# Performance work log

Measured on AMD Instinct MI355X. Metric: run time of the kernel, lower is better.

The kernel has to match this reference:

```python
import jax, jax.numpy as jnp
import numpy as np

N, E, F_IN, H, C = 50000, 800000, 128, 64, 10

def setup_inputs() -> dict:
    key = jax.random.key(0)
    ks = jax.random.split(key, 8)
    x = jax.random.normal(ks[0], (N, F_IN), dtype=jnp.float32)
    edge_index = jax.random.randint(ks[1], (2, E), 0, N, dtype=jnp.int32)
    edge_weight = jax.random.uniform(ks[2], (E,), dtype=jnp.float32)
    W1 = jax.random.normal(ks[3], (H, F_IN), dtype=jnp.float32) * 0.05
    W2 = jax.random.normal(ks[4], (H, H), dtype=jnp.float32) * 0.05
    W3 = jax.random.normal(ks[5], (C, H), dtype=jnp.float32) * 0.05
    b1 = jnp.zeros((H,), jnp.float32)
    b2 = jnp.zeros((H,), jnp.float32)
    b3 = jnp.zeros((C,), jnp.float32)
    return {"x": x, "edge_index": edge_index, "edge_weight": edge_weight,
            "W1": W1, "b1": b1, "W2": W2, "b2": b2, "W3": W3, "b3": b3}

def reference(x, edge_index, edge_weight, W1, b1, W2, b2, W3, b3):
    n = x.shape[0]
    row, col = edge_index[0], edge_index[1]
    # GCN symmetric normalization (add_self_loops=False): deg from edge weights on col
    deg = jax.ops.segment_sum(edge_weight, col, num_segments=n)  # [N]
    dinv = jnp.where(deg > 0, jax.lax.rsqrt(deg), 0.0)
    norm = dinv[row] * edge_weight * dinv[col]  # [E]

    def gcn_layer(h, W, b):
        h = h @ W.T                               # linear transform [N, out]
        msg = h[row] * norm[:, None]              # gather + scale   [E, out]
        agg = jax.ops.segment_sum(msg, col, num_segments=n)  # scatter-add [N, out]
        return agg + b

    h = gcn_layer(x, W1, b1)
    h = gcn_layer(h, W2, b2)
    logits = gcn_layer(h, W3, b3)
    soft = jax.nn.softmax(logits, axis=1)
    return logits, soft
```

## Files before the change

kernel.cpp:

```cpp
#include <hip/hip_runtime.h>
#include <hip/hip_fp16.h>

#define N_NODES 50000
#define N_EDGES 800000
#define F_IN    128
#define H_DIM   64
#define C_DIM   10
#define CPAD    16
#define CAP     48
#define BLOCK   256
#define BIN_NODES 256
#define NBINS   196
#define STRIDE  4480
#define E_BLK   2048
#define ABLOCKS ((N_EDGES + E_BLK - 1) / E_BLK)
#define DGB     (N_NODES / 16)
#define WB      ((N_NODES * 64) / 256)
#define POISON  ((int)0xAAAAAAAA)

__device__ __forceinline__ int unbase(int v) {
    return ((unsigned)v < 65536u) ? v : v - POISON;
}

__device__ __forceinline__ int   prow(unsigned v) { return (int)(v >> 16); }
__device__ __forceinline__ float pw(unsigned v)   {
    return __half2float(__ushort_as_half((unsigned short)(v & 0xFFFFu)));
}

__global__ __launch_bounds__(256) void k_binA(const int* __restrict__ rows,
                                              const int* __restrict__ cols,
                                              const float* __restrict__ ew,
                                              const float* __restrict__ W1,
                                              const float* __restrict__ b1,
                                              const float* __restrict__ W2,
                                              const float* __restrict__ b2,
                                              const float* __restrict__ W3,
                                              int* __restrict__ bucketCnt,
                                              unsigned* __restrict__ regionA,
                                              unsigned short* __restrict__ regionC,
                                              float* __restrict__ T2g,
                                              float* __restrict__ v1g,
                                              float* __restrict__ v2g) {
    const int tid = threadIdx.x;
    if (blockIdx.x < ABLOCKS) {
        __shared__ unsigned       sA[E_BLK];
        __shared__ unsigned short sC[E_BLK];
        __shared__ int hcnt[NBINS];
        __shared__ int lbase[NBINS];
        __shared__ int gb[NBINS];
        for (int i = tid; i < NBINS; i += BLOCK) hcnt[i] = 0;
        __syncthreads();

        const int e0 = blockIdx.x * E_BLK;
        unsigned rw[8];
        unsigned cl[8];
#pragma unroll
        for (int j = 0; j < 8; ++j) {
            int e = e0 + j * BLOCK + tid;
            if (e < N_EDGES) {
                int   c = cols[e];
                int   r = rows[e];
                float w = ew[e];
                rw[j] = ((unsigned)r << 16) | (unsigned)__half_as_ushort(__float2half(w));
                int lr = atomicAdd(&hcnt[c >> 8], 1);
                cl[j] = (unsigned)c | ((unsigned)lr << 16);
            } else {
                cl[j] = 0xFFFFFFFFu;
            }
        }
        __syncthreads();

        if (tid < 64) {
            int run = 0;
            for (int base = 0; base < NBINS; base += 64) {
                int i = base + tid;
                int v = (i < NBINS) ? hcnt[i] : 0;
                int s = v;
#pragma unroll
                for (int off = 1; off < 64; off <<= 1) {
                    int t = __shfl_up(s, off);
                    if (tid >= off) s += t;
                }
                if (i < NBINS) lbase[i] = run + s - v;
                run += __shfl(s, 63);
            }
        }
        __syncthreads();

#pragma unroll
        for (int j = 0; j < 8; ++j) {
            if (cl[j] != 0xFFFFFFFFu) {
                int c  = (int)(cl[j] & 0xFFFFu);
                int lr = (int)(cl[j] >> 16);
                int pos = lbase[c >> 8] + lr;
                sA[pos] = rw[j];
                sC[pos] = (unsigned short)c;
            }
        }
        if (tid < NBINS) gb[tid] = unbase(atomicAdd(&bucketCnt[tid], hcnt[tid]));
        __syncthreads();

        const int total = lbase[NBINS - 1] + hcnt[NBINS - 1];
        for (int i = tid; i < total; i += BLOCK) {
            int c = sC[i];
            int b = c >> 8;
            int gpos = gb[b] + (i - lbase[b]);
            if (gpos < STRIDE) {
                size_t p = (size_t)b * STRIDE + gpos;
                regionA[p] = sA[i];
                regionC[p] = (unsigned short)c;
            }
        }
        return;
    }

    __shared__ float u[C_DIM * H_DIM];
    for (int idx = tid; idx < C_DIM * H_DIM; idx += BLOCK) {
        int c = idx >> 6, j = idx & 63;
        float a = 0.f;
#pragma unroll
        for (int k = 0; k < H_DIM; ++k) a += W3[c * H_DIM + k] * W2[k * H_DIM + j];
        u[idx] = a;
    }
    __syncthreads();
    for (int idx = tid; idx < C_DIM * F_IN; idx += BLOCK) {
        int c = idx >> 7, f = idx & 127;
        float a = 0.f;
#pragma unroll
        for (int k = 0; k < H_DIM; ++k) a += u[c * H_DIM + k] * W1[k * F_IN + f];
        T2g[idx] = a;
    }
    if (tid < C_DIM) {
        float a = 0.f, b = 0.f;
#pragma unroll
        for (int k = 0; k < H_DIM; ++k) {
            a += u[tid * H_DIM + k] * b1[k];
            b += W3[tid * H_DIM + k] * b2[k];
        }
        v1g[tid] = a;
        v2g[tid] = b;
    }
}

__global__ __launch_bounds__(256) void k_binB(const int* __restrict__ bucketCnt,
                                              const unsigned* __restrict__ regionA,
                                              const unsigned short* __restrict__ regionC,
                                              float2* __restrict__ meta,
                                              unsigned* __restrict__ edata) {
    __shared__ unsigned sdata[BIN_NODES * CAP];
    __shared__ int   lcnt[BIN_NODES];
    __shared__ float wsum[BIN_NODES];
    const int tid = threadIdx.x;
    const int b   = blockIdx.x;
    if (tid < BIN_NODES) { lcnt[tid] = 0; wsum[tid] = 0.f; }
    __syncthreads();

    int tot = unbase(bucketCnt[b]);
    if (tot > STRIDE) tot = STRIDE;
    const size_t segBase = (size_t)b * STRIDE;
    for (int i = tid; i < tot; i += BLOCK) {
        unsigned e = regionA[segBase + i];
        int nl = (int)regionC[segBase + i] - b * BIN_NODES;
        int r = atomicAdd(&lcnt[nl], 1);
        if (r < CAP) sdata[nl * CAP + r] = e;
        atomicAdd(&wsum[nl], pw(e));
    }
    __syncthreads();

    const int n0 = b * BIN_NODES;
    const int nvalid = min(N_NODES - n0, BIN_NODES);
    if (tid < nvalid) {
        int c0 = min(lcnt[tid], CAP);
        int cp = (c0 + 15) & ~15;
        if (cp > CAP) cp = CAP;
        for (int r = c0; r < cp; ++r) sdata[tid * CAP + r] = 0u;
        float d = wsum[tid];
        meta[n0 + tid] = make_float2(d > 0.f ? rsqrtf(d) : 0.f, (float)cp);
    }
    __syncthreads();

    int4* dst = reinterpret_cast<int4*>(edata + (size_t)n0 * CAP);
    const int4* src = reinterpret_cast<const int4*>(sdata);
    const int nvec = nvalid * CAP / 4;
    for (int i = tid; i < nvec; i += BLOCK) dst[i] = src[i];
}

__global__ __launch_bounds__(256) void k_dg(const float* __restrict__ x,
                                            const float* __restrict__ T2g,
                                            const float2* __restrict__ meta,
                                            __half* __restrict__ bufA) {
    __shared__ float ts[16 * 132];
    __shared__ float xs[16][132];
    const int tid = threadIdx.x;
    const int n0 = blockIdx.x * 16;

    for (int i = tid; i < 16 * F_IN; i += BLOCK) {
        int c = i >> 7;
        ts[c * 132 + (i & 127)] = (c < C_DIM) ? T2g[i] : 0.f;
    }
    for (int i = tid; i < 16 * 32; i += BLOCK) {
        int ln = i >> 5, f4 = i & 31;
        float4 v = reinterpret_cast<const float4*>(x)[(n0 + ln) * 32 + f4];
        *reinterpret_cast<float4*>(&xs[ln][f4 * 4]) = v;
    }
    __syncthreads();

    const int g = tid >> 4;
    const int c = tid & 15;
    const int n = n0 + g;
    const float di = meta[n].x;

    const float4* tsv = reinterpret_cast<const float4*>(&ts[c * 132]);
    const float4* xv  = reinterpret_cast<const float4*>(&xs[g][0]);
    float a = 0.f;
#pragma unroll 8
    for (int f4 = 0; f4 < 32; ++f4) {
        float4 xx = xv[f4], tt = tsv[f4];
        a += xx.x * tt.x + xx.y * tt.y + xx.z * tt.z + xx.w * tt.w;
    }
    float outv = (c < C_DIM) ? a * di : (c == 10 ? di : 0.f);
    bufA[n * CPAD + c] = __float2half(outv);
}

__global__ __launch_bounds__(256) void k_gather(const float2* __restrict__ meta,
                                                const unsigned* __restrict__ edata,
                                                const __half* __restrict__ zin,
                                                __half* __restrict__ zout) {
    int n = (blockIdx.x * 256 + threadIdx.x) >> 6;
    if (n >= N_NODES) return;
    int lane = threadIdx.x & 63;
    int sub = lane >> 4, c = lane & 15;
    float2 m = meta[n];
    float di = m.x;
    int iters = ((int)m.y) >> 4;
    int base = n * CAP + sub;
    float acc = 0.f;
#pragma unroll
    for (int i = 0; i < 3; ++i) {
        if (i < iters) {
            int k = base + i * 16;
            unsigned e0 = edata[k];
            unsigned e1 = edata[k + 4];
            unsigned e2 = edata[k + 8];
            unsigned e3 = edata[k + 12];
            acc += pw(e0) * __half2float(zin[prow(e0) * CPAD + c]);
            acc += pw(e1) * __half2float(zin[prow(e1) * CPAD + c]);
            acc += pw(e2) * __half2float(zin[prow(e2) * CPAD + c]);
            acc += pw(e3) * __half2float(zin[prow(e3) * CPAD + c]);
        }
    }
    acc += __shfl_xor(acc, 32);
    acc += __shfl_xor(acc, 16);
    if (lane < 16) zout[n * CPAD + lane] = __float2half(acc * di * di);
}

__global__ __launch_bounds__(256) void k_final(const float2* __restrict__ meta,
                                               const unsigned* __restrict__ edata,
                                               const __half* __restrict__ zin,
                                               const __half* __restrict__ s1buf,
                                               const float* __restrict__ v1,
                                               const float* __restrict__ v2,
                                               const float* __restrict__ b3,
                                               float* __restrict__ logits,
                                               float* __restrict__ soft) {
    int n = (blockIdx.x * 256 + threadIdx.x) >> 6;
    if (n >= N_NODES) return;
    int lane = threadIdx.x & 63;
    int sub = lane >> 4, c = lane & 15;
    float2 m = meta[n];
    float di = m.x;
    int iters = ((int)m.y) >> 4;
    int base = n * CAP + sub;
    float acc = 0.f;
#pragma unroll
    for (int i = 0; i < 3; ++i) {
        if (i < iters) {
            int k = base + i * 16;
            unsigned e0 = edata[k];
            unsigned e1 = edata[k + 4];
            unsigned e2 = edata[k + 8];
            unsigned e3 = edata[k + 12];
            acc += pw(e0) * __half2float(zin[prow(e0) * CPAD + c]);
            acc += pw(e1) * __half2float(zin[prow(e1) * CPAD + c]);
            acc += pw(e2) * __half2float(zin[prow(e2) * CPAD + c]);
            acc += pw(e3) * __half2float(zin[prow(e3) * CPAD + c]);
        }
    }
    acc += __shfl_xor(acc, 32);
    acc += __shfl_xor(acc, 16);

    float r  = di > 0.f ? 1.0f / di : 0.f;
    float a1 = __half2float(s1buf[n * CPAD + 10]) * r;
    float a2 = __half2float(zin[n * CPAD + 10]) * r;
    float l = (c < C_DIM) ? di * acc + a2 * v1[c] + a1 * v2[c] + b3[c] : -1e30f;
    float mx = l;
#pragma unroll
    for (int d = 8; d >= 1; d >>= 1) mx = fmaxf(mx, __shfl_xor(mx, d));
    float ev = (c < C_DIM) ? __expf(l - mx) : 0.f;
    float s = ev;
#pragma unroll
    for (int d = 8; d >= 1; d >>= 1) s += __shfl_xor(s, d);
    if (lane < C_DIM) {
        logits[n * C_DIM + lane] = l;
        soft[n * C_DIM + lane]   = ev / s;
    }
}

extern "C" void kernel_launch(void* const* d_in, const int* in_sizes, int n_in,
                              void* d_out, int out_size, void* d_ws, size_t ws_size,
                              hipStream_t stream) {
    const float* x  = (const float*)d_in[0];
    const int*   ei = (const int*)d_in[1];
    const float* ew = (const float*)d_in[2];
    const float* W1 = (const float*)d_in[3];
    const float* b1 = (const float*)d_in[4];
    const float* W2 = (const float*)d_in[5];
    const float* b2 = (const float*)d_in[6];
    const float* W3 = (const float*)d_in[7];
    const float* b3 = (const float*)d_in[8];
    const int* rows = ei;
    const int* cols = ei + N_EDGES;

    char* ws = (char*)d_ws;
    size_t off = 0;
    auto alloc = [&](size_t bytes) { void* q = ws + off; off += (bytes + 15) & ~size_t(15); return q; };

    float2*         meta      = (float2*)         alloc((size_t)N_NODES * 8);
    __half*         bufA      = (__half*)         alloc((size_t)N_NODES * CPAD * 2);
    __half*         bufB      = (__half*)         alloc((size_t)N_NODES * CPAD * 2);
    float*          T2g       = (float*)          alloc(C_DIM * F_IN * 4);
    float*          v1        = (float*)          alloc(64);
    float*          v2        = (float*)          alloc(64);
    int*            bucketCnt = (int*)            alloc(NBINS * 4);
    unsigned*       regionA   = (unsigned*)       alloc((size_t)NBINS * STRIDE * 4);
    unsigned short* regionC   = (unsigned short*) alloc((size_t)NBINS * STRIDE * 2);
    unsigned*       edata     = (unsigned*)       alloc((size_t)N_NODES * CAP * 4);

    float* logits = (float*)d_out;
    float* soft   = logits + N_NODES * C_DIM;

    k_binA<<<ABLOCKS + 1, 256, 0, stream>>>(rows, cols, ew, W1, b1, W2, b2, W3,
                                            bucketCnt, regionA, regionC, T2g, v1, v2);
    k_binB<<<NBINS, 256, 0, stream>>>(bucketCnt, regionA, regionC, meta, edata);
    k_dg<<<DGB, 256, 0, stream>>>(x, T2g, meta, bufA);
    k_gather<<<WB, 256, 0, stream>>>(meta, edata, bufA, bufB);
    k_gather<<<WB, 256, 0, stream>>>(meta, edata, bufB, bufA);
    k_final<<<WB, 256, 0, stream>>>(meta, edata, bufA, bufB, v1, v2, b3,
                                    logits, soft);
}
```

Measured before the change: 166.7 us.

## Split binB into quarter-bin blocks and vectorize gather with half2 loads

The bucket-compaction kernel now launches four blocks per bin. Each block scans the whole bin but keeps only the 64 nodes in its quarter, which raises parallelism and shrinks shared memory per block at the cost of reading each bin's data four times. The gather and final kernels switch to 8 edge lanes × 8 half2 feature lanes, with uint2 edge loads and a three-step shuffle reduction, which halves the scalar zin loads. The final softmax now writes float2 pairs. It also skips the bucket atomic when a bin's local count is zero.

```diff
diff --git a/kernel.cpp b/kernel.cpp
--- a/kernel.cpp
+++ b/kernel.cpp
@@ -11,6 +11,7 @@
 #define BLOCK   256
 #define BIN_NODES 256
 #define NBINS   196
+#define QN      64
 #define STRIDE  4480
 #define E_BLK   2048
 #define ABLOCKS ((N_EDGES + E_BLK - 1) / E_BLK)
@@ -97,7 +98,8 @@
                 sC[pos] = (unsigned short)c;
             }
         }
-        if (tid < NBINS) gb[tid] = unbase(atomicAdd(&bucketCnt[tid], hcnt[tid]));
+        if (tid < NBINS && hcnt[tid] > 0)
+            gb[tid] = unbase(atomicAdd(&bucketCnt[tid], hcnt[tid]));
         __syncthreads();
 
         const int total = lbase[NBINS - 1] + hcnt[NBINS - 1];
@@ -147,28 +149,34 @@
                                               const unsigned short* __restrict__ regionC,
                                               float2* __restrict__ meta,
                                               unsigned* __restrict__ edata) {
-    __shared__ unsigned sdata[BIN_NODES * CAP];
-    __shared__ int   lcnt[BIN_NODES];
-    __shared__ float wsum[BIN_NODES];
+    __shared__ unsigned sdata[QN * CAP];
+    __shared__ int   lcnt[QN];
+    __shared__ float wsum[QN];
     const int tid = threadIdx.x;
-    const int b   = blockIdx.x;
-    if (tid < BIN_NODES) { lcnt[tid] = 0; wsum[tid] = 0.f; }
+    const int b   = blockIdx.x >> 2;
+    const int q   = blockIdx.x & 3;
+    const int n0  = b * BIN_NODES + q * QN;
+    if (n0 >= N_NODES) return;
+    if (tid < QN) { lcnt[tid] = 0; wsum[tid] = 0.f; }
     __syncthreads();
 
     int tot = unbase(bucketCnt[b]);
     if (tot > STRIDE) tot = STRIDE;
     const size_t segBase = (size_t)b * STRIDE;
+    const int lo = q * QN, hi = lo + QN;
     for (int i = tid; i < tot; i += BLOCK) {
+        int cl = (int)regionC[segBase + i] - b * BIN_NODES;
         unsigned e = regionA[segBase + i];
-        int nl = (int)regionC[segBase + i] - b * BIN_NODES;
-        int r = atomicAdd(&lcnt[nl], 1);
-        if (r < CAP) sdata[nl * CAP + r] = e;
-        atomicAdd(&wsum[nl], pw(e));
-    }
-    __syncthreads();
-
-    const int n0 = b * BIN_NODES;
-    const int nvalid = min(N_NODES - n0, BIN_NODES);
+        if (cl >= lo && cl < hi) {
+            int nl = cl - lo;
+            int r = atomicAdd(&lcnt[nl], 1);
+            if (r < CAP) sdata[nl * CAP + r] = e;
+            atomicAdd(&wsum[nl], pw(e));
+        }
+    }
+    __syncthreads();
+
+    const int nvalid = min(N_NODES - n0, QN);
     if (tid < nvalid) {
         int c0 = min(lcnt[tid], CAP);
         int cp = (c0 + 15) & ~15;
@@ -181,7 +189,7 @@
 
     int4* dst = reinterpret_cast<int4*>(edata + (size_t)n0 * CAP);
     const int4* src = reinterpret_cast<const int4*>(sdata);
-    const int nvec = nvalid * CAP / 4;
+    const int nvec = nvalid * (CAP / 4);
     for (int i = tid; i < nvec; i += BLOCK) dst[i] = src[i];
 }
 
@@ -228,30 +236,40 @@
                                                 __half* __restrict__ zout) {
     int n = (blockIdx.x * 256 + threadIdx.x) >> 6;
     if (n >= N_NODES) return;
-    int lane = threadIdx.x & 63;
-    int sub = lane >> 4, c = lane & 15;
+    const int lane = threadIdx.x & 63;
+    const int sub = lane >> 3;
+    const int c2  = lane & 7;
     float2 m = meta[n];
-    float di = m.x;
-    int iters = ((int)m.y) >> 4;
-    int base = n * CAP + sub;
-    float acc = 0.f;
+    const float di = m.x;
+    const int iters = ((int)m.y) >> 4;
+    const uint2* bp = reinterpret_cast<const uint2*>(edata + n * CAP) + sub;
+    float ax = 0.f, ay = 0.f;
 #pragma unroll
     for (int i = 0; i < 3; ++i) {
         if (i < iters) {
-            int k = base + i * 16;
-            unsigned e0 = edata[k];
-            unsigned e1 = edata[k + 4];
-            unsigned e2 = edata[k + 8];
-            unsigned e3 = edata[k + 12];
-            acc += pw(e0) * __half2float(zin[prow(e0) * CPAD + c]);
-            acc += pw(e1) * __half2float(zin[prow(e1) * CPAD + c]);
-            acc += pw(e2) * __half2float(zin[prow(e2) * CPAD + c]);
-            acc += pw(e3) * __half2float(zin[prow(e3) * CPAD + c]);
-        }
-    }
-    acc += __shfl_xor(acc, 32);
-    acc += __shfl_xor(acc, 16);
-    if (lane < 16) zout[n * CPAD + lane] = __float2half(acc * di * di);
+            uint2 e = bp[i * 8];
+            {
+                float2 z = __half22float2(
+                    reinterpret_cast<const __half2*>(zin + prow(e.x) * CPAD)[c2]);
+                float w = pw(e.x);
+                ax += w * z.x; ay += w * z.y;
+            }
+            {
+                float2 z = __half22float2(
+                    reinterpret_cast<const __half2*>(zin + prow(e.y) * CPAD)[c2]);
+                float w = pw(e.y);
+                ax += w * z.x; ay += w * z.y;
+            }
+        }
+    }
+    ax += __shfl_xor(ax, 8);  ay += __shfl_xor(ay, 8);
+    ax += __shfl_xor(ax, 16); ay += __shfl_xor(ay, 16);
+    ax += __shfl_xor(ax, 32); ay += __shfl_xor(ay, 32);
+    if (lane < 8) {
+        float s = di * di;
+        reinterpret_cast<__half2*>(zout + n * CPAD)[lane] =
+            __floats2half2_rn(ax * s, ay * s);
+    }
 }
 
 __global__ __launch_bounds__(256) void k_final(const float2* __restrict__ meta,
@@ -265,44 +283,61 @@
                                                float* __restrict__ soft) {
     int n = (blockIdx.x * 256 + threadIdx.x) >> 6;
     if (n >= N_NODES) return;
-    int lane = threadIdx.x & 63;
-    int sub = lane >> 4, c = lane & 15;
+    const int lane = threadIdx.x & 63;
+    const int sub = lane >> 3;
+    const int c2  = lane & 7;
     float2 m = meta[n];
-    float di = m.x;
-    int iters = ((int)m.y) >> 4;
-    int base = n * CAP + sub;
-    float acc = 0.f;
+    const float di = m.x;
+    const int iters = ((int)m.y) >> 4;
+    const uint2* bp = reinterpret_cast<const uint2*>(edata + n * CAP) + sub;
+    float ax = 0.f, ay = 0.f;
 #pragma unroll
     for (int i = 0; i < 3; ++i) {
         if (i < iters) {
-            int k = base + i * 16;
-            unsigned e0 = edata[k];
-            unsigned e1 = edata[k + 4];
-            unsigned e2 = edata[k + 8];
-            unsigned e3 = edata[k + 12];
-            acc += pw(e0) * __half2float(zin[prow(e0) * CPAD + c]);
-            acc += pw(e1) * __half2float(zin[prow(e1) * CPAD + c]);
-            acc += pw(e2) * __half2float(zin[prow(e2) * CPAD + c]);
-            acc += pw(e3) * __half2float(zin[prow(e3) * CPAD + c]);
-        }
-    }
-    acc += __shfl_xor(acc, 32);
-    acc += __shfl_xor(acc, 16);
-
-    float r  = di > 0.f ? 1.0f / di : 0.f;
-    float a1 = __half2float(s1buf[n * CPAD + 10]) * r;
-    float a2 = __half2float(zin[n * CPAD + 10]) * r;
-    float l = (c < C_DIM) ? di * acc + a2 * v1[c] + a1 * v2[c] + b3[c] : -1e30f;
-    float mx = l;
-#pragma unroll
-    for (int d = 8; d >= 1; d >>= 1) mx = fmaxf(mx, __shfl_xor(mx, d));
-    float ev = (c < C_DIM) ? __expf(l - mx) : 0.f;
-    float s = ev;
-#pragma unroll
-    for (int d = 8; d >= 1; d >>= 1) s += __shfl_xor(s, d);
-    if (lane < C_DIM) {
-        logits[n * C_DIM + lane] = l;
-        soft[n * C_DIM + lane]   = ev / s;
+            uint2 e = bp[i * 8];
+            {
+                float2 z = __half22float2(
+                    reinterpret_cast<const __half2*>(zin + prow(e.x) * CPAD)[c2]);
+                float w = pw(e.x);
+                ax += w * z.x; ay += w * z.y;
+            }
+            {
+                float2 z = __half22float2(
+                    reinterpret_cast<const __half2*>(zin + prow(e.y) * CPAD)[c2]);
+                float w = pw(e.y);
+                ax += w * z.x; ay += w * z.y;
+            }
+        }
+    }
+    ax += __shfl_xor(ax, 8);  ay += __shfl_xor(ay, 8);
+    ax += __shfl_xor(ax, 16); ay += __shfl_xor(ay, 16);
+    ax += __shfl_xor(ax, 32); ay += __shfl_xor(ay, 32);
+
+    const float r  = di > 0.f ? 1.0f / di : 0.f;
+    const float a1 = __half2float(s1buf[n * CPAD + 10]) * r;
+    const float a2 = __half2float(zin[n * CPAD + 10]) * r;
+    float l0 = -1e30f, l1 = -1e30f;
+    if (c2 < 5) {
+        float2 w1 = reinterpret_cast<const float2*>(v1)[c2];
+        float2 w2 = reinterpret_cast<const float2*>(v2)[c2];
+        float2 bb = reinterpret_cast<const float2*>(b3)[c2];
+        l0 = di * ax + a2 * w1.x + a1 * w2.x + bb.x;
+        l1 = di * ay + a2 * w1.y + a1 * w2.y + bb.y;
+    }
+    float mx = fmaxf(l0, l1);
+    mx = fmaxf(mx, __shfl_xor(mx, 1));
+    mx = fmaxf(mx, __shfl_xor(mx, 2));
+    mx = fmaxf(mx, __shfl_xor(mx, 4));
+    float e0 = (c2 < 5) ? __expf(l0 - mx) : 0.f;
+    float e1 = (c2 < 5) ? __expf(l1 - mx) : 0.f;
+    float s = e0 + e1;
+    s += __shfl_xor(s, 1);
+    s += __shfl_xor(s, 2);
+    s += __shfl_xor(s, 4);
+    if (lane < 5) {
+        float inv = 1.0f / s;
+        reinterpret_cast<float2*>(logits + (size_t)n * C_DIM)[lane] = make_float2(l0, l1);
+        reinterpret_cast<float2*>(soft   + (size_t)n * C_DIM)[lane] = make_float2(e0 * inv, e1 * inv);
     }
 }
 
@@ -339,12 +374,12 @@
     float* logits = (float*)d_out;
     float* soft   = logits + N_NODES * C_DIM;
 
-    k_binA<<<ABLOCKS + 1, 256, 0, stream>>>(rows, cols, ew, W1, b1, W2, b2, W3,
-                                            bucketCnt, regionA, regionC, T2g, v1, v2);
-    k_binB<<<NBINS, 256, 0, stream>>>(bucketCnt, regionA, regionC, meta, edata);
-    k_dg<<<DGB, 256, 0, stream>>>(x, T2g, meta, bufA);
-    k_gather<<<WB, 256, 0, stream>>>(meta, edata, bufA, bufB);
-    k_gather<<<WB, 256, 0, stream>>>(meta, edata, bufB, bufA);
-    k_final<<<WB, 256, 0, stream>>>(meta, edata, bufA, bufB, v1, v2, b3,
-                                    logits, soft);
-}
+    k_binA<<<ABLOCKS + 1, BLOCK, 0, stream>>>(rows, cols, ew, W1, b1, W2, b2, W3,
+                                              bucketCnt, regionA, regionC, T2g, v1, v2);
+    k_binB<<<NBINS * 4, BLOCK, 0, stream>>>(bucketCnt, regionA, regionC, meta, edata);
+    k_dg<<<DGB, BLOCK, 0, stream>>>(x, T2g, meta, bufA);
+    k_gather<<<WB, BLOCK, 0, stream>>>(meta, edata, bufA, bufB);
+    k_gather<<<WB, BLOCK, 0, stream>>>(meta, edata, bufB, bufA);
+    k_final<<<WB, BLOCK, 0, stream>>>(meta, edata, bufA, bufB, v1, v2, b3,
+                                      logits, soft);
+}
```

After: 167.9 us. About the same (+0.7%).
